# Optimization experiments

Hardware: AMD Instinct MI355X
Metric: run time of the kernel (lower is better)

## Reference

```python
import jax, jax.numpy as jnp
import numpy as np

B, R, H = 64, 32, 1024  # batch, num_rounds, lstm_hidden_size
IN = 2 * H              # GatedTrans in_dim
EPS = 1e-12             # F.normalize eps


def _gated(x, Wy, by, Wg, bg):
    # GatedTrans: tanh branch * leaky_relu branch (slope 0.01, torch default)
    return jnp.tanh(x @ Wy + by) * jax.nn.leaky_relu(x @ Wg + bg, 0.01)


def setup_inputs() -> dict:
    key = jax.random.key(0)
    ks = jax.random.split(key, 12)
    s_in = 1.0 / np.sqrt(IN)
    s_h = 1.0 / np.sqrt(H)
    return {
        "hist": jax.random.normal(ks[0], (B, R, IN), jnp.float32),
        "ques": jax.random.normal(ks[1], (B, R, IN), jnp.float32),
        "W_hy": jax.random.normal(ks[2], (IN, H), jnp.float32) * s_in,
        "b_hy": jnp.zeros((H,), jnp.float32),
        "W_hg": jax.random.normal(ks[3], (IN, H), jnp.float32) * s_in,
        "b_hg": jnp.zeros((H,), jnp.float32),
        "W_qy": jax.random.normal(ks[4], (IN, H), jnp.float32) * s_in,
        "b_qy": jnp.zeros((H,), jnp.float32),
        "W_qg": jax.random.normal(ks[5], (IN, H), jnp.float32) * s_in,
        "b_qg": jnp.zeros((H,), jnp.float32),
        "W_att": jax.random.normal(ks[6], (H,), jnp.float32) * s_h,
        "b_att": jnp.zeros((), jnp.float32),
    }


def reference(hist, ques, W_hy, b_hy, W_hg, b_hg, W_qy, b_qy, W_qg, b_qg, W_att, b_att):
    hist_embed = _gated(hist, W_hy, b_hy, W_hg, b_hg)   # [B, R, H]
    ques_embed = _gated(ques, W_qy, b_qy, W_qg, b_qg)   # [B, R, H]
    # broadcast outer product over rounds: [B, Rq, Rh, H]
    att_embed = ques_embed[:, :, None, :] * hist_embed[:, None, :, :]
    norm = jnp.sqrt(jnp.sum(att_embed * att_embed, axis=-1, keepdims=True))
    att_embed = att_embed / jnp.maximum(norm, EPS)       # F.normalize(p=2)
    scores = att_embed @ W_att + b_att                   # [B, Rq, Rh]
    att = jax.nn.softmax(scores, axis=-1)
    tril = jnp.tril(jnp.ones((R, R), jnp.float32))       # causal round mask
    att_masked = att * tril
    att_masked = att_masked / jnp.sum(att_masked, axis=-1, keepdims=True)
    # weighted sum over hist rounds: [B, Rq, 2H]
    feat = jnp.einsum("bqh,bhd->bqd", att_masked, hist)
    return feat
```

## Files before the change

### kernel.cpp

```cpp
#include <hip/hip_runtime.h>
#include <cstdint>

#define IN_DIM 2048
#define H_DIM  1024
#define BROWS  2048
#define BATCH  64
#define ROUNDS 32

typedef __bf16 bf16x8 __attribute__((ext_vector_type(8)));
typedef float  f32x4  __attribute__((ext_vector_type(4)));
typedef unsigned short u16;

__device__ __forceinline__ u16 f2bf(float f) {
    unsigned int u = __float_as_uint(f);
    u += 0x7FFFu + ((u >> 16) & 1u);
    return (u16)(u >> 16);
}
__device__ __forceinline__ float bf2f(u16 v) {
    return __uint_as_float(((unsigned int)v) << 16);
}

__device__ __forceinline__ void async_ld16(const void* g, void* l) {
    __builtin_amdgcn_global_load_lds(
        (__attribute__((address_space(1))) void*)(uintptr_t)g,
        (__attribute__((address_space(3))) void*)(unsigned int)(uintptr_t)l,
        16, 0, 0);
}

__global__ __launch_bounds__(256) void prep(
    const float* __restrict__ hist, const float* __restrict__ ques,
    u16* __restrict__ xh, u16* __restrict__ xq,
    const float* __restrict__ why, const float* __restrict__ whg,
    const float* __restrict__ wqy, const float* __restrict__ wqg,
    u16* __restrict__ oh, u16* __restrict__ oq)
{
    int idx = blockIdx.x;
    if (idx < 4096) {
        int i = idx * 256 + threadIdx.x;
        const float4* h4 = (const float4*)hist;
        const float4* q4 = (const float4*)ques;
        float4 a = h4[i], b = q4[i];
        ushort4 oa, ob;
        oa.x = f2bf(a.x); oa.y = f2bf(a.y); oa.z = f2bf(a.z); oa.w = f2bf(a.w);
        ob.x = f2bf(b.x); ob.y = f2bf(b.y); ob.z = f2bf(b.z); ob.w = f2bf(b.w);
        ((ushort4*)xh)[i] = oa;
        ((ushort4*)xq)[i] = ob;
        return;
    }
    __shared__ float t[32][33];
    int zz = idx - 4096;
    int z = zz >> 12, rem = zz & 4095;
    const float* Y = z == 0 ? why : wqy;
    const float* G = z == 0 ? whg : wqg;
    u16* O = z == 0 ? oh : oq;
    int n0 = (rem & 63) * 32, k0 = (rem >> 6) * 32;
    int tx = threadIdx.x & 31, ty = threadIdx.x >> 5;
    const float* S = (tx < 16) ? Y : G;
    int sc = (n0 >> 1) + (tx & 15);
    #pragma unroll
    for (int r = 0; r < 4; r++)
        t[ty + 8*r][tx] = S[(size_t)(k0 + ty + 8*r) * H_DIM + sc];
    __syncthreads();
    #pragma unroll
    for (int r = 0; r < 4; r++)
        O[(size_t)(n0 + ty + 8*r) * IN_DIM + k0 + tx] = f2bf(t[tx][ty + 8*r]);
}

__global__ __launch_bounds__(256) void gemm_act(
    const u16* __restrict__ xh, const u16* __restrict__ xq,
    const u16* __restrict__ wth, const u16* __restrict__ wtq,
    const float* __restrict__ bhy, const float* __restrict__ bhg,
    const float* __restrict__ bqy, const float* __restrict__ bqg,
    u16* __restrict__ eh, u16* __restrict__ eq)
{
    int z = blockIdx.z;
    const u16* A  = z == 0 ? xh : xq;
    const u16* Bt = z == 0 ? wth : wtq;
    const float* by = z == 0 ? bhy : bqy;
    const float* bg = z == 0 ? bhg : bqg;
    u16* E = z == 0 ? eh : eq;

    __shared__ __align__(16) u16 As[128 * 128];
    __shared__ __align__(16) u16 Bs[128 * 128];

    int tid = threadIdx.x;
    int wave = tid >> 6, lane = tid & 63;
    int lane15 = lane & 15, quad = lane >> 4;
    int wm = (wave >> 1) * 64, wn = (wave & 1) * 64;
    int m0 = blockIdx.y * 128, n0 = blockIdx.x * 128;

    f32x4 acc[4][4];
    #pragma unroll
    for (int i = 0; i < 4; i++)
        #pragma unroll
        for (int j = 0; j < 4; j++) acc[i][j] = (f32x4){0.f, 0.f, 0.f, 0.f};

    int srow[8], skc[8], scb[8];
    #pragma unroll
    for (int r2 = 0; r2 < 8; r2++) {
        int cbase = r2 * 256 + wave * 64;
        int cs = cbase + lane;
        int row = cs >> 4, s = cs & 15;
        srow[r2] = row; skc[r2] = s ^ (row & 15); scb[r2] = cbase;
    }

    for (int kt = 0; kt < IN_DIM; kt += 128) {
        #pragma unroll
        for (int r2 = 0; r2 < 8; r2++) {
            async_ld16(A  + (size_t)(m0 + srow[r2]) * IN_DIM + kt + skc[r2] * 8, &As[scb[r2] * 8]);
            async_ld16(Bt + (size_t)(n0 + srow[r2]) * IN_DIM + kt + skc[r2] * 8, &Bs[scb[r2] * 8]);
        }
        __syncthreads();
        #pragma unroll
        for (int ks = 0; ks < 4; ks++) {
            bf16x8 af[4], bfv[4];
            #pragma unroll
            for (int i = 0; i < 4; i++) {
                int row = wm + i * 16 + lane15;
                int s = (ks * 4 + quad) ^ (row & 15);
                af[i] = *(const bf16x8*)&As[row * 128 + s * 8];
            }
            #pragma unroll
            for (int j = 0; j < 4; j++) {
                int row = wn + j * 16 + lane15;
                int s = (ks * 4 + quad) ^ (row & 15);
                bfv[j] = *(const bf16x8*)&Bs[row * 128 + s * 8];
            }
            #pragma unroll
            for (int i = 0; i < 4; i++)
                #pragma unroll
                for (int j = 0; j < 4; j++)
                    acc[i][j] = __builtin_amdgcn_mfma_f32_16x16x32_bf16(af[i], bfv[j], acc[i][j], 0, 0, 0);
        }
        __syncthreads();
    }

    int n0w = n0 + wn;
    #pragma unroll
    for (int jp = 0; jp < 2; jp++) {
        int hc = (n0w >> 1) + jp * 16 + lane15;
        float vy = by[hc], vg = bg[hc];
        #pragma unroll
        for (int i = 0; i < 4; i++) {
            #pragma unroll
            for (int r = 0; r < 4; r++) {
                int row = m0 + wm + i * 16 + quad * 4 + r;
                float y = tanhf(acc[i][2 * jp][r] + vy);
                float g = acc[i][2 * jp + 1][r] + vg;
                E[(size_t)row * H_DIM + hc] = f2bf(y * (g > 0.f ? g : 0.01f * g));
            }
        }
    }
}

__global__ __launch_bounds__(256) void score_feat(
    const u16* __restrict__ eh, const u16* __restrict__ eq,
    const float* __restrict__ hist, const float* __restrict__ watt,
    const float* __restrict__ batt, float* __restrict__ out)
{
    int idx = blockIdx.x;
    int b = idx & 63, q = idx >> 6;
    int tid = threadIdx.x, wave = tid >> 6, lane = tid & 63;
    __shared__ float sw[32], swn[32];

    const u16* qe = eq + (size_t)(b * ROUNDS + q) * H_DIM;
    float uw[16], u2[16];
    #pragma unroll
    for (int c = 0; c < 2; c++) {
        uint4 pk = ((const uint4*)qe)[lane + 64 * c];
        float4 w0 = ((const float4*)watt)[(lane + 64 * c) * 2];
        float4 w1 = ((const float4*)watt)[(lane + 64 * c) * 2 + 1];
        unsigned int ws[4] = {pk.x, pk.y, pk.z, pk.w};
        float wf[8] = {w0.x, w0.y, w0.z, w0.w, w1.x, w1.y, w1.z, w1.w};
        #pragma unroll
        for (int e = 0; e < 4; e++) {
            float lo = __uint_as_float(ws[e] << 16);
            float hi = __uint_as_float(ws[e] & 0xFFFF0000u);
            uw[c * 8 + 2 * e]     = lo * wf[2 * e];
            u2[c * 8 + 2 * e]     = lo * lo;
            uw[c * 8 + 2 * e + 1] = hi * wf[2 * e + 1];
            u2[c * 8 + 2 * e + 1] = hi * hi;
        }
    }
    for (int h = wave; h <= q; h += 4) {
        const u16* he = eh + (size_t)(b * ROUNDS + h) * H_DIM;
        float num = 0.f, nrm = 0.f;
        #pragma unroll
        for (int c = 0; c < 2; c++) {
            uint4 pk = ((const uint4*)he)[lane + 64 * c];
            unsigned int vs[4] = {pk.x, pk.y, pk.z, pk.w};
            #pragma unroll
            for (int e = 0; e < 4; e++) {
                float lo = __uint_as_float(vs[e] << 16);
                float hi = __uint_as_float(vs[e] & 0xFFFF0000u);
                num += uw[c * 8 + 2 * e] * lo + uw[c * 8 + 2 * e + 1] * hi;
                nrm += u2[c * 8 + 2 * e] * lo * lo + u2[c * 8 + 2 * e + 1] * hi * hi;
            }
        }
        #pragma unroll
        for (int off = 32; off > 0; off >>= 1) {
            num += __shfl_down(num, off);
            nrm += __shfl_down(nrm, off);
        }
        if (lane == 0)
            sw[h] = num / fmaxf(sqrtf(nrm), 1e-12f) + batt[0];
    }
    __syncthreads();
    if (tid == 0) {
        float mx = -1e30f;
        for (int h = 0; h <= q; h++) mx = fmaxf(mx, sw[h]);
        float zs = 0.f;
        for (int h = 0; h <= q; h++) { float e = expf(sw[h] - mx); swn[h] = e; zs += e; }
        float inv = 1.f / zs;
        for (int h = 0; h <= q; h++) swn[h] *= inv;
    }
    __syncthreads();
    const float4* hb = (const float4*)(hist + (size_t)b * ROUNDS * IN_DIM);
    float4* ob = (float4*)(out + (size_t)(b * ROUNDS + q) * IN_DIM);
    #pragma unroll
    for (int d0 = 0; d0 < 2; d0++) {
        int d = tid + d0 * 256;
        float4 a = {0.f, 0.f, 0.f, 0.f};
        for (int h = 0; h <= q; h++) {
            float w = swn[h];
            float4 x = hb[h * 512 + d];
            a.x += w * x.x; a.y += w * x.y; a.z += w * x.z; a.w += w * x.w;
        }
        ob[d] = a;
    }
}

extern "C" void kernel_launch(void* const* d_in, const int* in_sizes, int n_in,
                              void* d_out, int out_size, void* d_ws, size_t ws_size,
                              hipStream_t stream) {
    const float* hist = (const float*)d_in[0];
    const float* ques = (const float*)d_in[1];
    const float* Why  = (const float*)d_in[2];
    const float* bhy  = (const float*)d_in[3];
    const float* Whg  = (const float*)d_in[4];
    const float* bhg  = (const float*)d_in[5];
    const float* Wqy  = (const float*)d_in[6];
    const float* bqy  = (const float*)d_in[7];
    const float* Wqg  = (const float*)d_in[8];
    const float* bqg  = (const float*)d_in[9];
    const float* watt = (const float*)d_in[10];
    const float* batt = (const float*)d_in[11];
    float* out = (float*)d_out;

    char* w = (char*)d_ws;
    u16* Xh  = (u16*)w;
    u16* Xq  = Xh  + (size_t)BROWS * IN_DIM;
    u16* WtH = Xq  + (size_t)BROWS * IN_DIM;
    u16* WtQ = WtH + (size_t)IN_DIM * IN_DIM;
    u16* Eh  = WtQ + (size_t)IN_DIM * IN_DIM;
    u16* Eq  = Eh  + (size_t)BROWS * H_DIM;

    prep<<<12288, 256, 0, stream>>>(hist, ques, Xh, Xq, Why, Whg, Wqy, Wqg, WtH, WtQ);
    gemm_act<<<dim3(16, 16, 2), 256, 0, stream>>>(Xh, Xq, WtH, WtQ,
                                                  bhy, bhg, bqy, bqg, Eh, Eq);
    score_feat<<<2048, 256, 0, stream>>>(Eh, Eq, hist, watt, batt, out);
}
```

Baseline: 189.0 us.

## Double-buffer GEMM LDS tiles with BK=64 to overlap loads and MFMA

Splits the K tile from 128 into two 64-wide halves held in two LDS buffers, so the async global-to-LDS load of the next half is issued before the MFMA compute on the current half. The XOR swizzle changes to 8 chunks per row. The goal is to hide global load latency behind compute rather than fully serializing load, barrier and compute. The LDS footprint stays the same. The second half's load is only waited on by the next barrier, so correctness depends on that barrier draining the async loads.

```diff
diff --git a/kernel.cpp b/kernel.cpp
--- a/kernel.cpp
+++ b/kernel.cpp
@@ -15,9 +15,6 @@
     unsigned int u = __float_as_uint(f);
     u += 0x7FFFu + ((u >> 16) & 1u);
     return (u16)(u >> 16);
-}
-__device__ __forceinline__ float bf2f(u16 v) {
-    return __uint_as_float(((unsigned int)v) << 16);
 }
 
 __device__ __forceinline__ void async_ld16(const void* g, void* l) {
@@ -80,8 +77,8 @@
     const float* bg = z == 0 ? bhg : bqg;
     u16* E = z == 0 ? eh : eq;
 
-    __shared__ __align__(16) u16 As[128 * 128];
-    __shared__ __align__(16) u16 Bs[128 * 128];
+    __shared__ __align__(16) u16 As[2][128 * 64];
+    __shared__ __align__(16) u16 Bs[2][128 * 64];
 
     int tid = threadIdx.x;
     int wave = tid >> 6, lane = tid & 63;
@@ -95,45 +92,59 @@
         #pragma unroll
         for (int j = 0; j < 4; j++) acc[i][j] = (f32x4){0.f, 0.f, 0.f, 0.f};
 
-    int srow[8], skc[8], scb[8];
-    #pragma unroll
-    for (int r2 = 0; r2 < 8; r2++) {
+    int srow[4], skc[4], scb[4];
+    #pragma unroll
+    for (int r2 = 0; r2 < 4; r2++) {
         int cbase = r2 * 256 + wave * 64;
         int cs = cbase + lane;
-        int row = cs >> 4, s = cs & 15;
-        srow[r2] = row; skc[r2] = s ^ (row & 15); scb[r2] = cbase;
-    }
-
+        int row = cs >> 3, s = cs & 7;
+        srow[r2] = row; skc[r2] = s ^ (row & 7); scb[r2] = cbase;
+    }
+
+    #define STAGE(buf, kt)                                                                   \
+        _Pragma("unroll")                                                                    \
+        for (int r2 = 0; r2 < 4; r2++) {                                                     \
+            async_ld16(A  + (size_t)(m0 + srow[r2]) * IN_DIM + (kt) + skc[r2] * 8,           \
+                       &As[buf][scb[r2] * 8]);                                               \
+            async_ld16(Bt + (size_t)(n0 + srow[r2]) * IN_DIM + (kt) + skc[r2] * 8,           \
+                       &Bs[buf][scb[r2] * 8]);                                               \
+        }
+
+    #define COMPUTE(buf)                                                                     \
+        _Pragma("unroll")                                                                    \
+        for (int ks = 0; ks < 2; ks++) {                                                     \
+            bf16x8 af[4], bfv[4];                                                            \
+            _Pragma("unroll")                                                                \
+            for (int i = 0; i < 4; i++) {                                                    \
+                int row = wm + i * 16 + lane15;                                              \
+                int s = (ks * 4 + quad) ^ (row & 7);                                         \
+                af[i] = *(const bf16x8*)&As[buf][row * 64 + s * 8];                          \
+            }                                                                                \
+            _Pragma("unroll")                                                                \
+            for (int j = 0; j < 4; j++) {                                                    \
+                int row = wn + j * 16 + lane15;                                              \
+                int s = (ks * 4 + quad) ^ (row & 7);                                         \
+                bfv[j] = *(const bf16x8*)&Bs[buf][row * 64 + s * 8];                         \
+            }                                                                                \
+            _Pragma("unroll")                                                                \
+            for (int i = 0; i < 4; i++)                                                      \
+                _Pragma("unroll")                                                            \
+                for (int j = 0; j < 4; j++)                                                  \
+                    acc[i][j] = __builtin_amdgcn_mfma_f32_16x16x32_bf16(                     \
+                        af[i], bfv[j], acc[i][j], 0, 0, 0);                                  \
+        }
+
+    STAGE(0, 0)
     for (int kt = 0; kt < IN_DIM; kt += 128) {
-        #pragma unroll
-        for (int r2 = 0; r2 < 8; r2++) {
-            async_ld16(A  + (size_t)(m0 + srow[r2]) * IN_DIM + kt + skc[r2] * 8, &As[scb[r2] * 8]);
-            async_ld16(Bt + (size_t)(n0 + srow[r2]) * IN_DIM + kt + skc[r2] * 8, &Bs[scb[r2] * 8]);
-        }
         __syncthreads();
-        #pragma unroll
-        for (int ks = 0; ks < 4; ks++) {
-            bf16x8 af[4], bfv[4];
-            #pragma unroll
-            for (int i = 0; i < 4; i++) {
-                int row = wm + i * 16 + lane15;
-                int s = (ks * 4 + quad) ^ (row & 15);
-                af[i] = *(const bf16x8*)&As[row * 128 + s * 8];
-            }
-            #pragma unroll
-            for (int j = 0; j < 4; j++) {
-                int row = wn + j * 16 + lane15;
-                int s = (ks * 4 + quad) ^ (row & 15);
-                bfv[j] = *(const bf16x8*)&Bs[row * 128 + s * 8];
-            }
-            #pragma unroll
-            for (int i = 0; i < 4; i++)
-                #pragma unroll
-                for (int j = 0; j < 4; j++)
-                    acc[i][j] = __builtin_amdgcn_mfma_f32_16x16x32_bf16(af[i], bfv[j], acc[i][j], 0, 0, 0);
-        }
+        STAGE(1, kt + 64)
+        COMPUTE(0)
         __syncthreads();
-    }
+        if (kt + 128 < IN_DIM) STAGE(0, kt + 128)
+        COMPUTE(1)
+    }
+    #undef STAGE
+    #undef COMPUTE
 
     int n0w = n0 + wn;
     #pragma unroll
```

Result: no change. 189.0 us (+0.0%).

## Shrink GEMM M-tile, remap blocks for XCD locality, split score/feat stages

Applied to the files above, without the earlier changes.

The GEMM now uses 64x128 tiles launched as a 1D grid of 1024 blocks. The block index is remapped so that blocks sharing A rows and weight matrices land on the same XCD cluster, which should improve L2 reuse and raise block count for occupancy. The fused score+weighted-sum kernel is split in two: one kernel writes softmax weights to a workspace matrix, and a new feat kernel stages each batch's history chunk in LDS and reuses it across all 32 query rounds. This removes redundant global reads of hist at the cost of an extra launch and a workspace round trip. The feat kernel uses 72KB of shared memory per block, which limits occupancy.

```diff
diff --git a/kernel.cpp b/kernel.cpp
--- a/kernel.cpp
+++ b/kernel.cpp
@@ -15,9 +15,6 @@
     unsigned int u = __float_as_uint(f);
     u += 0x7FFFu + ((u >> 16) & 1u);
     return (u16)(u >> 16);
-}
-__device__ __forceinline__ float bf2f(u16 v) {
-    return __uint_as_float(((unsigned int)v) << 16);
 }
 
 __device__ __forceinline__ void async_ld16(const void* g, void* l) {
@@ -73,55 +70,68 @@
     const float* __restrict__ bqy, const float* __restrict__ bqg,
     u16* __restrict__ eh, u16* __restrict__ eq)
 {
-    int z = blockIdx.z;
+    int L = blockIdx.x;
+    int cluster = L & 7;
+    int slot = L >> 3;
+    int z  = cluster >> 2;
+    int my = (cluster & 3) * 8 + (slot >> 4);
+    int nx = slot & 15;
+    int m0 = my * 64, n0 = nx * 128;
+
     const u16* A  = z == 0 ? xh : xq;
     const u16* Bt = z == 0 ? wth : wtq;
     const float* by = z == 0 ? bhy : bqy;
     const float* bg = z == 0 ? bhg : bqg;
     u16* E = z == 0 ? eh : eq;
 
-    __shared__ __align__(16) u16 As[128 * 128];
+    __shared__ __align__(16) u16 As[64 * 128];
     __shared__ __align__(16) u16 Bs[128 * 128];
 
     int tid = threadIdx.x;
     int wave = tid >> 6, lane = tid & 63;
     int lane15 = lane & 15, quad = lane >> 4;
-    int wm = (wave >> 1) * 64, wn = (wave & 1) * 64;
-    int m0 = blockIdx.y * 128, n0 = blockIdx.x * 128;
-
-    f32x4 acc[4][4];
+    int wn = wave * 32;
+
+    f32x4 acc[4][2];
     #pragma unroll
     for (int i = 0; i < 4; i++)
         #pragma unroll
-        for (int j = 0; j < 4; j++) acc[i][j] = (f32x4){0.f, 0.f, 0.f, 0.f};
-
-    int srow[8], skc[8], scb[8];
-    #pragma unroll
-    for (int r2 = 0; r2 < 8; r2++) {
+        for (int j = 0; j < 2; j++) acc[i][j] = (f32x4){0.f, 0.f, 0.f, 0.f};
+
+    int srow[12], skc[12], sdst[12];
+    #pragma unroll
+    for (int r2 = 0; r2 < 12; r2++) {
         int cbase = r2 * 256 + wave * 64;
-        int cs = cbase + lane;
-        int row = cs >> 4, s = cs & 15;
-        srow[r2] = row; skc[r2] = s ^ (row & 15); scb[r2] = cbase;
+        int c = cbase + lane;
+        if (r2 < 4) {
+            int row = c >> 4, s = c & 15;
+            srow[r2] = row; skc[r2] = s ^ (row & 15); sdst[r2] = cbase * 8;
+        } else {
+            int c2 = c - 1024;
+            int row = c2 >> 4, s = c2 & 15;
+            srow[r2] = row; skc[r2] = s ^ (row & 15); sdst[r2] = (cbase - 1024) * 8;
+        }
     }
 
     for (int kt = 0; kt < IN_DIM; kt += 128) {
         #pragma unroll
-        for (int r2 = 0; r2 < 8; r2++) {
-            async_ld16(A  + (size_t)(m0 + srow[r2]) * IN_DIM + kt + skc[r2] * 8, &As[scb[r2] * 8]);
-            async_ld16(Bt + (size_t)(n0 + srow[r2]) * IN_DIM + kt + skc[r2] * 8, &Bs[scb[r2] * 8]);
-        }
+        for (int r2 = 0; r2 < 4; r2++)
+            async_ld16(A + (size_t)(m0 + srow[r2]) * IN_DIM + kt + skc[r2] * 8, &As[sdst[r2]]);
+        #pragma unroll
+        for (int r2 = 4; r2 < 12; r2++)
+            async_ld16(Bt + (size_t)(n0 + srow[r2]) * IN_DIM + kt + skc[r2] * 8, &Bs[sdst[r2]]);
         __syncthreads();
         #pragma unroll
         for (int ks = 0; ks < 4; ks++) {
-            bf16x8 af[4], bfv[4];
+            bf16x8 af[4], bfv[2];
             #pragma unroll
             for (int i = 0; i < 4; i++) {
-                int row = wm + i * 16 + lane15;
+                int row = i * 16 + lane15;
                 int s = (ks * 4 + quad) ^ (row & 15);
                 af[i] = *(const bf16x8*)&As[row * 128 + s * 8];
             }
             #pragma unroll
-            for (int j = 0; j < 4; j++) {
+            for (int j = 0; j < 2; j++) {
                 int row = wn + j * 16 + lane15;
                 int s = (ks * 4 + quad) ^ (row & 15);
                 bfv[j] = *(const bf16x8*)&Bs[row * 128 + s * 8];
@@ -129,34 +139,32 @@
             #pragma unroll
             for (int i = 0; i < 4; i++)
                 #pragma unroll
-                for (int j = 0; j < 4; j++)
+                for (int j = 0; j < 2; j++)
                     acc[i][j] = __builtin_amdgcn_mfma_f32_16x16x32_bf16(af[i], bfv[j], acc[i][j], 0, 0, 0);
         }
         __syncthreads();
     }
 
-    int n0w = n0 + wn;
-    #pragma unroll
-    for (int jp = 0; jp < 2; jp++) {
-        int hc = (n0w >> 1) + jp * 16 + lane15;
+    {
+        int hc = ((n0 + wn) >> 1) + lane15;
         float vy = by[hc], vg = bg[hc];
         #pragma unroll
         for (int i = 0; i < 4; i++) {
             #pragma unroll
             for (int r = 0; r < 4; r++) {
-                int row = m0 + wm + i * 16 + quad * 4 + r;
-                float y = tanhf(acc[i][2 * jp][r] + vy);
-                float g = acc[i][2 * jp + 1][r] + vg;
-                E[(size_t)row * H_DIM + hc] = f2bf(y * (g > 0.f ? g : 0.01f * g));
-            }
-        }
-    }
-}
-
-__global__ __launch_bounds__(256) void score_feat(
+                int row = m0 + i * 16 + quad * 4 + r;
+                float y2 = tanhf(acc[i][0][r] + vy);
+                float g = acc[i][1][r] + vg;
+                E[(size_t)row * H_DIM + hc] = f2bf(y2 * (g > 0.f ? g : 0.01f * g));
+            }
+        }
+    }
+}
+
+__global__ __launch_bounds__(256) void scores(
     const u16* __restrict__ eh, const u16* __restrict__ eq,
-    const float* __restrict__ hist, const float* __restrict__ watt,
-    const float* __restrict__ batt, float* __restrict__ out)
+    const float* __restrict__ watt, const float* __restrict__ batt,
+    float* __restrict__ wmat)
 {
     int idx = blockIdx.x;
     int b = idx & 63, q = idx >> 6;
@@ -215,18 +223,46 @@
         for (int h = 0; h <= q; h++) swn[h] *= inv;
     }
     __syncthreads();
+    if (tid <= q)
+        wmat[((size_t)(b * ROUNDS) + q) * ROUNDS + tid] = swn[tid];
+}
+
+__global__ __launch_bounds__(256) void feat(
+    const float* __restrict__ wmat, const float* __restrict__ hist,
+    float* __restrict__ out)
+{
+    int idx = blockIdx.x;
+    int b = idx & 63, chunk = idx >> 6;
+    int tid = threadIdx.x;
+    __shared__ float hs[32][512];
+    __shared__ float ws[32][32];
+
     const float4* hb = (const float4*)(hist + (size_t)b * ROUNDS * IN_DIM);
-    float4* ob = (float4*)(out + (size_t)(b * ROUNDS + q) * IN_DIM);
-    #pragma unroll
-    for (int d0 = 0; d0 < 2; d0++) {
-        int d = tid + d0 * 256;
+    #pragma unroll
+    for (int r = 0; r < 16; r++) {
+        int e = r * 256 + tid;
+        int h = e >> 7, c = e & 127;
+        float4 v = hb[h * 512 + chunk * 128 + c];
+        hs[h][c * 4 + 0] = v.x; hs[h][c * 4 + 1] = v.y;
+        hs[h][c * 4 + 2] = v.z; hs[h][c * 4 + 3] = v.w;
+    }
+    {
+        const float* wb = wmat + (size_t)b * ROUNDS * ROUNDS;
+        #pragma unroll
+        for (int r = 0; r < 4; r++) ((float*)ws)[r * 256 + tid] = wb[r * 256 + tid];
+    }
+    __syncthreads();
+
+    int col = tid & 127, qpar = tid >> 7;
+    float* ob = out + (size_t)b * ROUNDS * IN_DIM + chunk * 512 + col * 4;
+    for (int q = qpar; q < 32; q += 2) {
         float4 a = {0.f, 0.f, 0.f, 0.f};
         for (int h = 0; h <= q; h++) {
-            float w = swn[h];
-            float4 x = hb[h * 512 + d];
+            float w = ws[q][h];
+            const float4 x = *(const float4*)&hs[h][col * 4];
             a.x += w * x.x; a.y += w * x.y; a.z += w * x.z; a.w += w * x.w;
         }
-        ob[d] = a;
+        *(float4*)(ob + (size_t)q * IN_DIM) = a;
     }
 }
 
@@ -254,9 +290,10 @@
     u16* WtQ = WtH + (size_t)IN_DIM * IN_DIM;
     u16* Eh  = WtQ + (size_t)IN_DIM * IN_DIM;
     u16* Eq  = Eh  + (size_t)BROWS * H_DIM;
+    float* Wm = (float*)(Eq + (size_t)BROWS * H_DIM);
 
     prep<<<12288, 256, 0, stream>>>(hist, ques, Xh, Xq, Why, Whg, Wqy, Wqg, WtH, WtQ);
-    gemm_act<<<dim3(16, 16, 2), 256, 0, stream>>>(Xh, Xq, WtH, WtQ,
-                                                  bhy, bhg, bqy, bqg, Eh, Eq);
-    score_feat<<<2048, 256, 0, stream>>>(Eh, Eq, hist, watt, batt, out);
-}
+    gemm_act<<<1024, 256, 0, stream>>>(Xh, Xq, WtH, WtQ, bhy, bhg, bqy, bqg, Eh, Eq);
+    scores<<<2048, 256, 0, stream>>>(Eh, Eq, watt, batt, Wm);
+    feat<<<256, 256, 0, stream>>>(Wm, hist, out);
+}
```

Result: slower. 207.4 us (+9.8%).
